# Optimization experiments

Measured on AMD Instinct MI355X. Metric: run time of the kernel, lower is better.

## Reference

```python
import jax, jax.numpy as jnp
import numpy as np

ALPHA = 0.5
PATH_LEN = 7  # 1 start entity + 3 (module, entity) hops
NUM_ENTITIES = 200000
EMBED = 128
NUM_MOD = 64
HIDDEN = 512
OUT_DIM = 64
BATCH = 8192


def setup_inputs() -> dict:
    key = jax.random.key(0)
    ks = jax.random.split(key, 8)
    stdv = 1.0 / np.sqrt(EMBED)
    return {
        "entity_embeds": jax.random.normal(ks[0], (NUM_ENTITIES, EMBED), jnp.float32) * 0.05,
        "W_mods": jax.random.uniform(ks[1], (NUM_MOD, EMBED, EMBED), jnp.float32, -stdv, stdv),
        "W1": jax.random.normal(ks[2], (HIDDEN, EMBED), jnp.float32) * stdv,
        "b1": jax.random.normal(ks[3], (HIDDEN,), jnp.float32) * 0.01,
        "W2": jax.random.normal(ks[4], (OUT_DIM, HIDDEN), jnp.float32) * (1.0 / np.sqrt(HIDDEN)),
        "b2": jax.random.normal(ks[5], (OUT_DIM,), jnp.float32) * 0.01,
        "entity_ids": jax.random.randint(ks[6], (BATCH, 4), 0, NUM_ENTITIES, jnp.int64 if jax.config.jax_enable_x64 else jnp.int32),
        "module_ids": jax.random.randint(ks[7], (BATCH, 3), 0, NUM_MOD, jnp.int64 if jax.config.jax_enable_x64 else jnp.int32),
    }


def reference(entity_embeds, W_mods, W1, b1, W2, b2, entity_ids, module_ids):
    # Batched version of ModuleNet.forward over a batch of fixed-length-7 paths.
    x = entity_embeds[entity_ids[:, 0]]  # [B, E] start entity embedding
    bias = x
    for h in range(3):  # hops over (module_id, entity_id) pairs
        Wm = W_mods[module_ids[:, h]]          # [B, E, E] per-row weight gather
        bias = entity_embeds[entity_ids[:, h + 1]]  # [B, E]
        x = jax.nn.relu(jnp.einsum('boi,bi->bo', Wm, x) + bias)
    w = 1.0 / (PATH_LEN * ALPHA)
    out = (1.0 - w) * bias + w * x  # [B, E]
    # classifier: Linear -> ReLU -> Linear
    h1 = jax.nn.relu(out @ W1.T + b1)
    logits = h1 @ W2.T + b2  # [B, OUT_DIM]
    return logits
```

## Files before the change

kernel.cpp:

```cpp
#include <hip/hip_runtime.h>

namespace {

typedef short bf16x8 __attribute__((ext_vector_type(8)));
typedef float f32x4 __attribute__((ext_vector_type(4)));

constexpr int BATCH = 8192;
constexpr int NMOD  = 64;
constexpr int CAP   = 256;
constexpr int CSTR  = 16;
constexpr float WB  = 1.0f / (7.0f * 0.5f);

constexpr size_t OFF_WHI = 0;
constexpr size_t OFF_WLO = 524288;
constexpr size_t OFF_X0  = 1048576;
constexpr size_t OFF_X1  = 2097152;
constexpr size_t OFF_W1T = 3145728;
constexpr size_t OFF_W2T = 3211264;
constexpr size_t OFF_CNT = 3244032;
constexpr size_t OFF_BKT = 3247104;

__device__ __forceinline__ ushort f2bf(float x) {
  unsigned u = __builtin_bit_cast(unsigned, x);
  u += 0x7FFFu + ((u >> 16) & 1u);
  return (ushort)(u >> 16);
}
__device__ __forceinline__ float bf2f(ushort h) {
  return __builtin_bit_cast(float, ((unsigned)h) << 16);
}
__device__ __forceinline__ void cvt8(const float* v, bf16x8& hi, bf16x8& lo) {
#pragma unroll
  for (int j = 0; j < 8; ++j) {
    const float x = v[j];
    const ushort h = f2bf(x);
    hi[j] = (short)h;
    lo[j] = (short)f2bf(x - bf2f(h));
  }
}

__global__ __launch_bounds__(256) void k_prep(const float* __restrict__ Wm,
                                              const float* __restrict__ W1,
                                              const float* __restrict__ W2,
                                              const int* __restrict__ mids,
                                              float* __restrict__ ws) {
  __shared__ float t[64 * 129];
  const int bx = blockIdx.x;
  const int tid = threadIdx.x;
  if (bx < 512) {
    const size_t i8 = (size_t)bx * 256 + tid;
    float v[8];
    *(float4*)&v[0] = *(const float4*)&Wm[i8 * 8];
    *(float4*)&v[4] = *(const float4*)&Wm[i8 * 8 + 4];
    bf16x8 hi, lo;
    cvt8(v, hi, lo);
    *(bf16x8*)((ushort*)(ws + OFF_WHI) + i8 * 8) = hi;
    *(bf16x8*)((ushort*)(ws + OFF_WLO) + i8 * 8) = lo;
  } else if (bx < 520) {
    const int j = bx - 512;
    for (int e = tid; e < 64 * 32; e += 256) {
      const int r = e >> 5, i4 = e & 31;
      const float4 v = *(const float4*)&W1[(size_t)(j * 64 + r) * 128 + 4 * i4];
      float* d = &t[r * 129 + 4 * i4];
      d[0] = v.x; d[1] = v.y; d[2] = v.z; d[3] = v.w;
    }
    __syncthreads();
    float* W1T = ws + OFF_W1T;
    for (int e = tid; e < 128 * 16; e += 256) {
      const int i = e >> 4, r4 = e & 15;
      float4 v;
      v.x = t[(4 * r4 + 0) * 129 + i];
      v.y = t[(4 * r4 + 1) * 129 + i];
      v.z = t[(4 * r4 + 2) * 129 + i];
      v.w = t[(4 * r4 + 3) * 129 + i];
      *(float4*)&W1T[(size_t)i * 512 + j * 64 + 4 * r4] = v;
    }
  } else if (bx < 528) {
    const int j = bx - 520;
    float* t2 = t;
    for (int e = tid; e < 64 * 16; e += 256) {
      const int o = e >> 4, k4 = e & 15;
      const float4 v = *(const float4*)&W2[(size_t)o * 512 + j * 64 + 4 * k4];
      float* d = &t2[o * 65 + 4 * k4];
      d[0] = v.x; d[1] = v.y; d[2] = v.z; d[3] = v.w;
    }
    __syncthreads();
    float* W2T = ws + OFF_W2T;
    for (int e = tid; e < 64 * 16; e += 256) {
      const int k = e >> 4, o4 = e & 15;
      float4 v;
      v.x = t2[(4 * o4 + 0) * 65 + k];
      v.y = t2[(4 * o4 + 1) * 65 + k];
      v.z = t2[(4 * o4 + 2) * 65 + k];
      v.w = t2[(4 * o4 + 3) * 65 + k];
      *(float4*)&W2T[(size_t)(j * 64 + k) * 64 + 4 * o4] = v;
    }
  } else {
    const int idx = (bx - 528) * 256 + tid;
    if (idx < BATCH * 3) {
      const int b = idx / 3, h = idx - b * 3;
      const int m = mids[idx];
      int* cnt = (int*)(ws + OFF_CNT);
      int* bkt = (int*)(ws + OFF_BKT);
      const int pos = atomicAdd(&cnt[(h * NMOD + m) * CSTR], 1);
      bkt[(h * NMOD + m) * CAP + pos] = b;
    }
  }
}

template <int HOP>
__global__ __launch_bounds__(256, 2) void k_hop(const float* __restrict__ E,
                                                const int* __restrict__ eids,
                                                float* __restrict__ ws) {
  const int m = blockIdx.x >> 2, sl = blockIdx.x & 3;
  const int cn = ((const int*)(ws + OFF_CNT))[(HOP * NMOD + m) * CSTR];
  const int r0 = sl * 64;
  if (r0 >= cn) return;
  const int nr = min(64, cn - r0);

  __shared__ ushort wh[128 * 72];
  __shared__ ushort wl[128 * 72];
  __shared__ int rows[64], esrc[64], ebia[64];

  const int tid = threadIdx.x;
  const ushort* WhiG = (const ushort*)(ws + OFF_WHI) + (size_t)m * 16384;
  const ushort* WloG = (const ushort*)(ws + OFF_WLO) + (size_t)m * 16384;
  const int* bkt = (const int*)(ws + OFF_BKT) + (HOP * NMOD + m) * CAP + r0;
  const float* Xprev = ws + (HOP == 1 ? OFF_X0 : OFF_X1);
  float* Xnext = ws + (HOP == 1 ? OFF_X1 : OFF_X0);

  if (tid < 64) {
    const int b = bkt[tid < nr ? tid : 0];
    rows[tid] = b;
    esrc[tid] = (HOP == 0) ? eids[b * 4] : b;
    ebia[tid] = eids[b * 4 + HOP + 1];
  }

  const int w = tid >> 6, l = tid & 63;
  const int lg = l >> 4, lr = l & 15;
  const int g0 = (w & 1) * 2, f0 = (w >> 1) * 4;
  const float* xbase = (HOP == 0) ? E : Xprev;

  f32x4 acc[2][4] = {};

#pragma unroll
  for (int p = 0; p < 2; ++p) {
    __syncthreads();
    for (int e = tid; e < 128 * 8; e += 256) {
      const int c = e >> 3, s = e & 7;
      *(bf16x8*)&wh[c * 72 + s * 8] =
          *(const bf16x8*)&WhiG[(size_t)c * 128 + p * 64 + s * 8];
      *(bf16x8*)&wl[c * 72 + s * 8] =
          *(const bf16x8*)&WloG[(size_t)c * 128 + p * 64 + s * 8];
    }
    __syncthreads();

    bf16x8 ah[2][2], al[2][2];
#pragma unroll
    for (int g = 0; g < 2; ++g) {
      const int row = (g0 + g) * 16 + lr;
      const float* sp = xbase + (size_t)esrc[row] * 128;
#pragma unroll
      for (int s = 0; s < 2; ++s) {
        float v[8];
        const int k0 = p * 64 + s * 32 + lg * 8;
        *(float4*)&v[0] = *(const float4*)&sp[k0];
        *(float4*)&v[4] = *(const float4*)&sp[k0 + 4];
        cvt8(v, ah[g][s], al[g][s]);
      }
    }

#pragma unroll
    for (int f = 0; f < 4; ++f) {
      const int c = (f0 + f) * 16 + lr;
      bf16x8 bh[2], bl[2];
#pragma unroll
      for (int s = 0; s < 2; ++s) {
        bh[s] = *(const bf16x8*)&wh[c * 72 + s * 32 + lg * 8];
        bl[s] = *(const bf16x8*)&wl[c * 72 + s * 32 + lg * 8];
      }
#pragma unroll
      for (int g = 0; g < 2; ++g) {
#pragma unroll
        for (int s = 0; s < 2; ++s) {
          acc[g][f] = __builtin_amdgcn_mfma_f32_16x16x32_bf16(
              ah[g][s], bh[s], acc[g][f], 0, 0, 0);
          acc[g][f] = __builtin_amdgcn_mfma_f32_16x16x32_bf16(
              al[g][s], bh[s], acc[g][f], 0, 0, 0);
          acc[g][f] = __builtin_amdgcn_mfma_f32_16x16x32_bf16(
              ah[g][s], bl[s], acc[g][f], 0, 0, 0);
        }
      }
    }
  }

#pragma unroll
  for (int g = 0; g < 2; ++g) {
#pragma unroll
    for (int q = 0; q < 4; ++q) {
      const int row = (g0 + g) * 16 + lg * 4 + q;
      if (row < nr) {
        const int b = rows[row];
        const float* bp = E + (size_t)ebia[row] * 128;
        float* op = Xnext + (size_t)b * 128;
#pragma unroll
        for (int f = 0; f < 4; ++f) {
          const int col = (f0 + f) * 16 + lr;
          const float bias = bp[col];
          float v = fmaxf(acc[g][f][q] + bias, 0.f);
          if (HOP == 2) v = (1.f - WB) * bias + WB * v;
          op[col] = v;
        }
      }
    }
  }
}

constexpr int HS = 516;
__global__ __launch_bounds__(256) void k_mlp(const float* __restrict__ b1,
                                             const float* __restrict__ b2,
                                             float* __restrict__ ws,
                                             float* __restrict__ out) {
  __shared__ float xs[16 * 129];
  __shared__ float hs[16 * HS];
  __shared__ float part[4 * 1024];
  const int tid = threadIdx.x;
  const int row0 = blockIdx.x * 16;
  const float* X = ws + OFF_X0;
  const float* W1T = ws + OFF_W1T;
  const float* W2T = ws + OFF_W2T;

  for (int e = tid; e < 16 * 32; e += 256) {
    const int row = e >> 5, i4 = e & 31;
    *(float4*)&xs[row * 129 + 4 * i4] =
        *(const float4*)&X[(size_t)(row0 + row) * 128 + 4 * i4];
  }
  __syncthreads();

  const int wv = tid >> 6, ln = tid & 63;
#pragma unroll
  for (int pass = 0; pass < 2; ++pass) {
    float acc[4][4] = {};
    const float* Wp = W1T + pass * 256 + 4 * ln;
#pragma unroll 4
    for (int k = 0; k < 128; ++k) {
      const float4 w = *(const float4*)&Wp[(size_t)k * 512];
      const float a0 = xs[(wv * 4 + 0) * 129 + k];
      const float a1 = xs[(wv * 4 + 1) * 129 + k];
      const float a2 = xs[(wv * 4 + 2) * 129 + k];
      const float a3 = xs[(wv * 4 + 3) * 129 + k];
      acc[0][0] = fmaf(a0, w.x, acc[0][0]); acc[0][1] = fmaf(a0, w.y, acc[0][1]);
      acc[0][2] = fmaf(a0, w.z, acc[0][2]); acc[0][3] = fmaf(a0, w.w, acc[0][3]);
      acc[1][0] = fmaf(a1, w.x, acc[1][0]); acc[1][1] = fmaf(a1, w.y, acc[1][1]);
      acc[1][2] = fmaf(a1, w.z, acc[1][2]); acc[1][3] = fmaf(a1, w.w, acc[1][3]);
      acc[2][0] = fmaf(a2, w.x, acc[2][0]); acc[2][1] = fmaf(a2, w.y, acc[2][1]);
      acc[2][2] = fmaf(a2, w.z, acc[2][2]); acc[2][3] = fmaf(a2, w.w, acc[2][3]);
      acc[3][0] = fmaf(a3, w.x, acc[3][0]); acc[3][1] = fmaf(a3, w.y, acc[3][1]);
      acc[3][2] = fmaf(a3, w.z, acc[3][2]); acc[3][3] = fmaf(a3, w.w, acc[3][3]);
    }
    const float4 bb = *(const float4*)&b1[pass * 256 + 4 * ln];
#pragma unroll
    for (int r = 0; r < 4; ++r) {
      float4 o;
      o.x = fmaxf(acc[r][0] + bb.x, 0.f);
      o.y = fmaxf(acc[r][1] + bb.y, 0.f);
      o.z = fmaxf(acc[r][2] + bb.z, 0.f);
      o.w = fmaxf(acc[r][3] + bb.w, 0.f);
      *(float4*)&hs[(wv * 4 + r) * HS + pass * 256 + 4 * ln] = o;
    }
  }
  __syncthreads();

  const int lr = ln >> 4, lc = ln & 15;
  float acc2[4][4] = {};
  const float* W2p = W2T + (size_t)wv * 128 * 64 + 4 * lc;
#pragma unroll 4
  for (int kk = 0; kk < 128; ++kk) {
    const int k = wv * 128 + kk;
    const float4 w = *(const float4*)&W2p[(size_t)kk * 64];
    const float a0 = hs[(lr * 4 + 0) * HS + k];
    const float a1 = hs[(lr * 4 + 1) * HS + k];
    const float a2 = hs[(lr * 4 + 2) * HS + k];
    const float a3 = hs[(lr * 4 + 3) * HS + k];
    acc2[0][0] = fmaf(a0, w.x, acc2[0][0]); acc2[0][1] = fmaf(a0, w.y, acc2[0][1]);
    acc2[0][2] = fmaf(a0, w.z, acc2[0][2]); acc2[0][3] = fmaf(a0, w.w, acc2[0][3]);
    acc2[1][0] = fmaf(a1, w.x, acc2[1][0]); acc2[1][1] = fmaf(a1, w.y, acc2[1][1]);
    acc2[1][2] = fmaf(a1, w.z, acc2[1][2]); acc2[1][3] = fmaf(a1, w.w, acc2[1][3]);
    acc2[2][0] = fmaf(a2, w.x, acc2[2][0]); acc2[2][1] = fmaf(a2, w.y, acc2[2][1]);
    acc2[2][2] = fmaf(a2, w.z, acc2[2][2]); acc2[2][3] = fmaf(a2, w.w, acc2[2][3]);
    acc2[3][0] = fmaf(a3, w.x, acc2[3][0]); acc2[3][1] = fmaf(a3, w.y, acc2[3][1]);
    acc2[3][2] = fmaf(a3, w.z, acc2[3][2]); acc2[3][3] = fmaf(a3, w.w, acc2[3][3]);
  }
#pragma unroll
  for (int r = 0; r < 4; ++r) {
    float4 pv;
    pv.x = acc2[r][0]; pv.y = acc2[r][1]; pv.z = acc2[r][2]; pv.w = acc2[r][3];
    *(float4*)&part[wv * 1024 + (lr * 4 + r) * 64 + 4 * lc] = pv;
  }
  __syncthreads();

  {
    const int r = tid >> 4, cf = tid & 15;
    float4 s = *(const float4*)&part[r * 64 + 4 * cf];
#pragma unroll
    for (int w = 1; w < 4; ++w) {
      const float4 t2 = *(const float4*)&part[w * 1024 + r * 64 + 4 * cf];
      s.x += t2.x; s.y += t2.y; s.z += t2.z; s.w += t2.w;
    }
    const float4 bb = *(const float4*)&b2[4 * cf];
    float4 o;
    o.x = s.x + bb.x; o.y = s.y + bb.y; o.z = s.z + bb.z; o.w = s.w + bb.w;
    *(float4*)&out[(size_t)(row0 + r) * 64 + 4 * cf] = o;
  }
}

}

extern "C" void kernel_launch(void* const* d_in, const int* in_sizes, int n_in,
                              void* d_out, int out_size, void* d_ws,
                              size_t ws_size, hipStream_t stream) {
  const float* E  = (const float*)d_in[0];
  const float* Wm = (const float*)d_in[1];
  const float* W1 = (const float*)d_in[2];
  const float* b1 = (const float*)d_in[3];
  const float* W2 = (const float*)d_in[4];
  const float* b2 = (const float*)d_in[5];
  const int* eids = (const int*)d_in[6];
  const int* mids = (const int*)d_in[7];
  float* out = (float*)d_out;
  float* ws = (float*)d_ws;

  (void)hipMemsetAsync((char*)d_ws + OFF_CNT * sizeof(float), 0,
                       192 * CSTR * sizeof(int), stream);
  k_prep<<<dim3(624), dim3(256), 0, stream>>>(Wm, W1, W2, mids, ws);
  k_hop<0><<<dim3(256), dim3(256), 0, stream>>>(E, eids, ws);
  k_hop<1><<<dim3(256), dim3(256), 0, stream>>>(E, eids, ws);
  k_hop<2><<<dim3(256), dim3(256), 0, stream>>>(E, eids, ws);
  k_mlp<<<dim3(512), dim3(256), 0, stream>>>(b1, b2, ws, out);
}
```

Baseline: 88.12 us.

## Move classifier MLP to split-bf16 MFMA and store hop activations as bf16 hi/lo

```diff
diff --git a/kernel.cpp b/kernel.cpp
--- a/kernel.cpp
+++ b/kernel.cpp
@@ -13,10 +13,14 @@
 
 constexpr size_t OFF_WHI = 0;
 constexpr size_t OFF_WLO = 524288;
-constexpr size_t OFF_X0  = 1048576;
-constexpr size_t OFF_X1  = 2097152;
-constexpr size_t OFF_W1T = 3145728;
-constexpr size_t OFF_W2T = 3211264;
+constexpr size_t OFF_XH0 = 1048576;
+constexpr size_t OFF_XL0 = 1572864;
+constexpr size_t OFF_XH1 = 2097152;
+constexpr size_t OFF_XL1 = 2621440;
+constexpr size_t OFF_W1H = 3145728;
+constexpr size_t OFF_W1L = 3178496;
+constexpr size_t OFF_W2H = 3211264;
+constexpr size_t OFF_W2L = 3227648;
 constexpr size_t OFF_CNT = 3244032;
 constexpr size_t OFF_BKT = 3247104;
 
@@ -43,59 +47,31 @@
                                               const float* __restrict__ W2,
                                               const int* __restrict__ mids,
                                               float* __restrict__ ws) {
-  __shared__ float t[64 * 129];
   const int bx = blockIdx.x;
   const int tid = threadIdx.x;
-  if (bx < 512) {
-    const size_t i8 = (size_t)bx * 256 + tid;
+  if (bx < 560) {
+    const float* src;
+    ushort *dh, *dl;
+    size_t i8;
+    if (bx < 512) {
+      src = Wm; dh = (ushort*)(ws + OFF_WHI); dl = (ushort*)(ws + OFF_WLO);
+      i8 = (size_t)bx * 256 + tid;
+    } else if (bx < 544) {
+      src = W1; dh = (ushort*)(ws + OFF_W1H); dl = (ushort*)(ws + OFF_W1L);
+      i8 = (size_t)(bx - 512) * 256 + tid;
+    } else {
+      src = W2; dh = (ushort*)(ws + OFF_W2H); dl = (ushort*)(ws + OFF_W2L);
+      i8 = (size_t)(bx - 544) * 256 + tid;
+    }
     float v[8];
-    *(float4*)&v[0] = *(const float4*)&Wm[i8 * 8];
-    *(float4*)&v[4] = *(const float4*)&Wm[i8 * 8 + 4];
+    *(float4*)&v[0] = *(const float4*)&src[i8 * 8];
+    *(float4*)&v[4] = *(const float4*)&src[i8 * 8 + 4];
     bf16x8 hi, lo;
     cvt8(v, hi, lo);
-    *(bf16x8*)((ushort*)(ws + OFF_WHI) + i8 * 8) = hi;
-    *(bf16x8*)((ushort*)(ws + OFF_WLO) + i8 * 8) = lo;
-  } else if (bx < 520) {
-    const int j = bx - 512;
-    for (int e = tid; e < 64 * 32; e += 256) {
-      const int r = e >> 5, i4 = e & 31;
-      const float4 v = *(const float4*)&W1[(size_t)(j * 64 + r) * 128 + 4 * i4];
-      float* d = &t[r * 129 + 4 * i4];
-      d[0] = v.x; d[1] = v.y; d[2] = v.z; d[3] = v.w;
-    }
-    __syncthreads();
-    float* W1T = ws + OFF_W1T;
-    for (int e = tid; e < 128 * 16; e += 256) {
-      const int i = e >> 4, r4 = e & 15;
-      float4 v;
-      v.x = t[(4 * r4 + 0) * 129 + i];
-      v.y = t[(4 * r4 + 1) * 129 + i];
-      v.z = t[(4 * r4 + 2) * 129 + i];
-      v.w = t[(4 * r4 + 3) * 129 + i];
-      *(float4*)&W1T[(size_t)i * 512 + j * 64 + 4 * r4] = v;
-    }
-  } else if (bx < 528) {
-    const int j = bx - 520;
-    float* t2 = t;
-    for (int e = tid; e < 64 * 16; e += 256) {
-      const int o = e >> 4, k4 = e & 15;
-      const float4 v = *(const float4*)&W2[(size_t)o * 512 + j * 64 + 4 * k4];
-      float* d = &t2[o * 65 + 4 * k4];
-      d[0] = v.x; d[1] = v.y; d[2] = v.z; d[3] = v.w;
-    }
-    __syncthreads();
-    float* W2T = ws + OFF_W2T;
-    for (int e = tid; e < 64 * 16; e += 256) {
-      const int k = e >> 4, o4 = e & 15;
-      float4 v;
-      v.x = t2[(4 * o4 + 0) * 65 + k];
-      v.y = t2[(4 * o4 + 1) * 65 + k];
-      v.z = t2[(4 * o4 + 2) * 65 + k];
-      v.w = t2[(4 * o4 + 3) * 65 + k];
-      *(float4*)&W2T[(size_t)(j * 64 + k) * 64 + 4 * o4] = v;
-    }
+    *(bf16x8*)&dh[i8 * 8] = hi;
+    *(bf16x8*)&dl[i8 * 8] = lo;
   } else {
-    const int idx = (bx - 528) * 256 + tid;
+    const int idx = (bx - 560) * 256 + tid;
     if (idx < BATCH * 3) {
       const int b = idx / 3, h = idx - b * 3;
       const int m = mids[idx];
@@ -125,8 +101,10 @@
   const ushort* WhiG = (const ushort*)(ws + OFF_WHI) + (size_t)m * 16384;
   const ushort* WloG = (const ushort*)(ws + OFF_WLO) + (size_t)m * 16384;
   const int* bkt = (const int*)(ws + OFF_BKT) + (HOP * NMOD + m) * CAP + r0;
-  const float* Xprev = ws + (HOP == 1 ? OFF_X0 : OFF_X1);
-  float* Xnext = ws + (HOP == 1 ? OFF_X1 : OFF_X0);
+  const ushort* XHp = (const ushort*)(ws + (HOP == 2 ? OFF_XH1 : OFF_XH0));
+  const ushort* XLp = (const ushort*)(ws + (HOP == 2 ? OFF_XL1 : OFF_XL0));
+  ushort* XHn = (ushort*)(ws + (HOP == 1 ? OFF_XH1 : OFF_XH0));
+  ushort* XLn = (ushort*)(ws + (HOP == 1 ? OFF_XL1 : OFF_XL0));
 
   if (tid < 64) {
     const int b = bkt[tid < nr ? tid : 0];
@@ -138,7 +116,6 @@
   const int w = tid >> 6, l = tid & 63;
   const int lg = l >> 4, lr = l & 15;
   const int g0 = (w & 1) * 2, f0 = (w >> 1) * 4;
-  const float* xbase = (HOP == 0) ? E : Xprev;
 
   f32x4 acc[2][4] = {};
 
@@ -158,14 +135,20 @@
 #pragma unroll
     for (int g = 0; g < 2; ++g) {
       const int row = (g0 + g) * 16 + lr;
-      const float* sp = xbase + (size_t)esrc[row] * 128;
 #pragma unroll
       for (int s = 0; s < 2; ++s) {
-        float v[8];
         const int k0 = p * 64 + s * 32 + lg * 8;
-        *(float4*)&v[0] = *(const float4*)&sp[k0];
-        *(float4*)&v[4] = *(const float4*)&sp[k0 + 4];
-        cvt8(v, ah[g][s], al[g][s]);
+        if (HOP == 0) {
+          const float* sp = E + (size_t)esrc[row] * 128;
+          float v[8];
+          *(float4*)&v[0] = *(const float4*)&sp[k0];
+          *(float4*)&v[4] = *(const float4*)&sp[k0 + 4];
+          cvt8(v, ah[g][s], al[g][s]);
+        } else {
+          const size_t xo = (size_t)esrc[row] * 128 + k0;
+          ah[g][s] = *(const bf16x8*)&XHp[xo];
+          al[g][s] = *(const bf16x8*)&XLp[xo];
+        }
       }
     }
 
@@ -201,116 +184,97 @@
       if (row < nr) {
         const int b = rows[row];
         const float* bp = E + (size_t)ebia[row] * 128;
-        float* op = Xnext + (size_t)b * 128;
+        const size_t ob = (size_t)b * 128;
 #pragma unroll
         for (int f = 0; f < 4; ++f) {
           const int col = (f0 + f) * 16 + lr;
           const float bias = bp[col];
           float v = fmaxf(acc[g][f][q] + bias, 0.f);
           if (HOP == 2) v = (1.f - WB) * bias + WB * v;
-          op[col] = v;
+          const ushort h = f2bf(v);
+          XHn[ob + col] = h;
+          XLn[ob + col] = f2bf(v - bf2f(h));
         }
       }
     }
   }
 }
 
-constexpr int HS = 516;
-__global__ __launch_bounds__(256) void k_mlp(const float* __restrict__ b1,
-                                             const float* __restrict__ b2,
-                                             float* __restrict__ ws,
-                                             float* __restrict__ out) {
-  __shared__ float xs[16 * 129];
-  __shared__ float hs[16 * HS];
-  __shared__ float part[4 * 1024];
+constexpr int HSTR = 520;
+__global__ __launch_bounds__(256, 2) void k_mlp(const float* __restrict__ b1,
+                                                const float* __restrict__ b2,
+                                                float* __restrict__ ws,
+                                                float* __restrict__ out) {
+  __shared__ ushort hh[16 * HSTR];
+  __shared__ ushort hl[16 * HSTR];
   const int tid = threadIdx.x;
   const int row0 = blockIdx.x * 16;
-  const float* X = ws + OFF_X0;
-  const float* W1T = ws + OFF_W1T;
-  const float* W2T = ws + OFF_W2T;
-
-  for (int e = tid; e < 16 * 32; e += 256) {
-    const int row = e >> 5, i4 = e & 31;
-    *(float4*)&xs[row * 129 + 4 * i4] =
-        *(const float4*)&X[(size_t)(row0 + row) * 128 + 4 * i4];
+  const ushort* XH = (const ushort*)(ws + OFF_XH0);
+  const ushort* XL = (const ushort*)(ws + OFF_XL0);
+  const ushort* W1H = (const ushort*)(ws + OFF_W1H);
+  const ushort* W1L = (const ushort*)(ws + OFF_W1L);
+  const ushort* W2H = (const ushort*)(ws + OFF_W2H);
+  const ushort* W2L = (const ushort*)(ws + OFF_W2L);
+
+  const int w = tid >> 6, l = tid & 63;
+  const int lg = l >> 4, lr = l & 15;
+
+  bf16x8 ah[4], al[4];
+#pragma unroll
+  for (int s = 0; s < 4; ++s) {
+    const size_t xo = (size_t)(row0 + lr) * 128 + s * 32 + lg * 8;
+    ah[s] = *(const bf16x8*)&XH[xo];
+    al[s] = *(const bf16x8*)&XL[xo];
+  }
+  f32x4 acc[8] = {};
+#pragma unroll
+  for (int f = 0; f < 8; ++f) {
+    const int c = w * 128 + f * 16 + lr;
+#pragma unroll
+    for (int s = 0; s < 4; ++s) {
+      const size_t wo = (size_t)c * 128 + s * 32 + lg * 8;
+      const bf16x8 bh = *(const bf16x8*)&W1H[wo];
+      const bf16x8 bl = *(const bf16x8*)&W1L[wo];
+      acc[f] = __builtin_amdgcn_mfma_f32_16x16x32_bf16(ah[s], bh, acc[f], 0, 0, 0);
+      acc[f] = __builtin_amdgcn_mfma_f32_16x16x32_bf16(al[s], bh, acc[f], 0, 0, 0);
+      acc[f] = __builtin_amdgcn_mfma_f32_16x16x32_bf16(ah[s], bl, acc[f], 0, 0, 0);
+    }
+  }
+#pragma unroll
+  for (int f = 0; f < 8; ++f) {
+    const int c = w * 128 + f * 16 + lr;
+    const float bb = b1[c];
+#pragma unroll
+    for (int q = 0; q < 4; ++q) {
+      const int r = lg * 4 + q;
+      const float v = fmaxf(acc[f][q] + bb, 0.f);
+      const ushort h = f2bf(v);
+      hh[r * HSTR + c] = h;
+      hl[r * HSTR + c] = f2bf(v - bf2f(h));
+    }
   }
   __syncthreads();
 
-  const int wv = tid >> 6, ln = tid & 63;
-#pragma unroll
-  for (int pass = 0; pass < 2; ++pass) {
-    float acc[4][4] = {};
-    const float* Wp = W1T + pass * 256 + 4 * ln;
+  f32x4 acc2 = {};
 #pragma unroll 4
-    for (int k = 0; k < 128; ++k) {
-      const float4 w = *(const float4*)&Wp[(size_t)k * 512];
-      const float a0 = xs[(wv * 4 + 0) * 129 + k];
-      const float a1 = xs[(wv * 4 + 1) * 129 + k];
-      const float a2 = xs[(wv * 4 + 2) * 129 + k];
-      const float a3 = xs[(wv * 4 + 3) * 129 + k];
-      acc[0][0] = fmaf(a0, w.x, acc[0][0]); acc[0][1] = fmaf(a0, w.y, acc[0][1]);
-      acc[0][2] = fmaf(a0, w.z, acc[0][2]); acc[0][3] = fmaf(a0, w.w, acc[0][3]);
-      acc[1][0] = fmaf(a1, w.x, acc[1][0]); acc[1][1] = fmaf(a1, w.y, acc[1][1]);
-      acc[1][2] = fmaf(a1, w.z, acc[1][2]); acc[1][3] = fmaf(a1, w.w, acc[1][3]);
-      acc[2][0] = fmaf(a2, w.x, acc[2][0]); acc[2][1] = fmaf(a2, w.y, acc[2][1]);
-      acc[2][2] = fmaf(a2, w.z, acc[2][2]); acc[2][3] = fmaf(a2, w.w, acc[2][3]);
-      acc[3][0] = fmaf(a3, w.x, acc[3][0]); acc[3][1] = fmaf(a3, w.y, acc[3][1]);
-      acc[3][2] = fmaf(a3, w.z, acc[3][2]); acc[3][3] = fmaf(a3, w.w, acc[3][3]);
-    }
-    const float4 bb = *(const float4*)&b1[pass * 256 + 4 * ln];
-#pragma unroll
-    for (int r = 0; r < 4; ++r) {
-      float4 o;
-      o.x = fmaxf(acc[r][0] + bb.x, 0.f);
-      o.y = fmaxf(acc[r][1] + bb.y, 0.f);
-      o.z = fmaxf(acc[r][2] + bb.z, 0.f);
-      o.w = fmaxf(acc[r][3] + bb.w, 0.f);
-      *(float4*)&hs[(wv * 4 + r) * HS + pass * 256 + 4 * ln] = o;
-    }
-  }
-  __syncthreads();
-
-  const int lr = ln >> 4, lc = ln & 15;
-  float acc2[4][4] = {};
-  const float* W2p = W2T + (size_t)wv * 128 * 64 + 4 * lc;
-#pragma unroll 4
-  for (int kk = 0; kk < 128; ++kk) {
-    const int k = wv * 128 + kk;
-    const float4 w = *(const float4*)&W2p[(size_t)kk * 64];
-    const float a0 = hs[(lr * 4 + 0) * HS + k];
-    const float a1 = hs[(lr * 4 + 1) * HS + k];
-    const float a2 = hs[(lr * 4 + 2) * HS + k];
-    const float a3 = hs[(lr * 4 + 3) * HS + k];
-    acc2[0][0] = fmaf(a0, w.x, acc2[0][0]); acc2[0][1] = fmaf(a0, w.y, acc2[0][1]);
-    acc2[0][2] = fmaf(a0, w.z, acc2[0][2]); acc2[0][3] = fmaf(a0, w.w, acc2[0][3]);
-    acc2[1][0] = fmaf(a1, w.x, acc2[1][0]); acc2[1][1] = fmaf(a1, w.y, acc2[1][1]);
-    acc2[1][2] = fmaf(a1, w.z, acc2[1][2]); acc2[1][3] = fmaf(a1, w.w, acc2[1][3]);
-    acc2[2][0] = fmaf(a2, w.x, acc2[2][0]); acc2[2][1] = fmaf(a2, w.y, acc2[2][1]);
-    acc2[2][2] = fmaf(a2, w.z, acc2[2][2]); acc2[2][3] = fmaf(a2, w.w, acc2[2][3]);
-    acc2[3][0] = fmaf(a3, w.x, acc2[3][0]); acc2[3][1] = fmaf(a3, w.y, acc2[3][1]);
-    acc2[3][2] = fmaf(a3, w.z, acc2[3][2]); acc2[3][3] = fmaf(a3, w.w, acc2[3][3]);
-  }
-#pragma unroll
-  for (int r = 0; r < 4; ++r) {
-    float4 pv;
-    pv.x = acc2[r][0]; pv.y = acc2[r][1]; pv.z = acc2[r][2]; pv.w = acc2[r][3];
-    *(float4*)&part[wv * 1024 + (lr * 4 + r) * 64 + 4 * lc] = pv;
-  }
-  __syncthreads();
-
-  {
-    const int r = tid >> 4, cf = tid & 15;
-    float4 s = *(const float4*)&part[r * 64 + 4 * cf];
-#pragma unroll
-    for (int w = 1; w < 4; ++w) {
-      const float4 t2 = *(const float4*)&part[w * 1024 + r * 64 + 4 * cf];
-      s.x += t2.x; s.y += t2.y; s.z += t2.z; s.w += t2.w;
-    }
-    const float4 bb = *(const float4*)&b2[4 * cf];
-    float4 o;
-    o.x = s.x + bb.x; o.y = s.y + bb.y; o.z = s.z + bb.z; o.w = s.w + bb.w;
-    *(float4*)&out[(size_t)(row0 + r) * 64 + 4 * cf] = o;
-  }
+  for (int s = 0; s < 16; ++s) {
+    const size_t wo = (size_t)(w * 16 + lr) * 512 + s * 32 + lg * 8;
+    const bf16x8 a2h = *(const bf16x8*)&W2H[wo];
+    const bf16x8 a2l = *(const bf16x8*)&W2L[wo];
+    const int ko = s * 32 + lg * 8;
+    const bf16x8 b2h = *(const bf16x8*)&hh[lr * HSTR + ko];
+    const bf16x8 b2l = *(const bf16x8*)&hl[lr * HSTR + ko];
+    acc2 = __builtin_amdgcn_mfma_f32_16x16x32_bf16(a2h, b2h, acc2, 0, 0, 0);
+    acc2 = __builtin_amdgcn_mfma_f32_16x16x32_bf16(a2l, b2h, acc2, 0, 0, 0);
+    acc2 = __builtin_amdgcn_mfma_f32_16x16x32_bf16(a2h, b2l, acc2, 0, 0, 0);
+  }
+  const float4 bb2 = *(const float4*)&b2[w * 16 + lg * 4];
+  float4 o;
+  o.x = acc2[0] + bb2.x;
+  o.y = acc2[1] + bb2.y;
+  o.z = acc2[2] + bb2.z;
+  o.w = acc2[3] + bb2.w;
+  *(float4*)&out[(size_t)(row0 + lr) * 64 + w * 16 + lg * 4] = o;
 }
 
 }
@@ -331,7 +295,7 @@
 
   (void)hipMemsetAsync((char*)d_ws + OFF_CNT * sizeof(float), 0,
                        192 * CSTR * sizeof(int), stream);
-  k_prep<<<dim3(624), dim3(256), 0, stream>>>(Wm, W1, W2, mids, ws);
+  k_prep<<<dim3(656), dim3(256), 0, stream>>>(Wm, W1, W2, mids, ws);
   k_hop<0><<<dim3(256), dim3(256), 0, stream>>>(E, eids, ws);
   k_hop<1><<<dim3(256), dim3(256), 0, stream>>>(E, eids, ws);
   k_hop<2><<<dim3(256), dim3(256), 0, stream>>>(E, eids, ws);
```

Measured after the change: 80.18 us. 9.0% less time.
